# Optimization experiments

Measured on AMD Instinct MI355X. Metric: run time of the kernel, lower is better.

Reference implementation:

```python
import jax, jax.numpy as jnp
import numpy as np

PI = np.pi


def _apply_1q(state, gate, wire, n):
    # state: [B, 2**n] complex64; gate: [2,2] (shared) or [B,2,2] (per-sample)
    # PennyLane convention: wire 0 is the most-significant bit of the state index.
    B = state.shape[0]
    left, right = 2 ** wire, 2 ** (n - wire - 1)
    s = state.reshape(B, left, 2, right)
    if gate.ndim == 2:
        s = jnp.einsum('kl,balr->bakr', gate, s)
    else:
        s = jnp.einsum('bkl,balr->bakr', gate, s)
    return s.reshape(B, -1)


def _apply_cz(state, wire, n):
    # CZ on (wire, wire+1): flip sign of |..11..> amplitudes
    B = state.shape[0]
    left, right = 2 ** wire, 2 ** (n - wire - 2)
    s = state.reshape(B, left, 2, 2, right)
    s = s.at[:, :, 1, 1, :].multiply(-1.0)
    return s.reshape(B, -1)


def _ry_batched(theta):
    # theta: [B] -> [B,2,2] complex RY(theta)
    h = 0.5 * theta
    c, s = jnp.cos(h), jnp.sin(h)
    g = jnp.stack([jnp.stack([c, -s], -1), jnp.stack([s, c], -1)], -2)
    return g.astype(jnp.complex64)


def _rot(phi, theta, omega):
    # Rot = RZ(omega) @ RY(theta) @ RZ(phi)
    c, s = jnp.cos(0.5 * theta), jnp.sin(0.5 * theta)
    e_mm = jnp.exp(-0.5j * (phi + omega))
    e_pm = jnp.exp(0.5j * (phi - omega))
    e_mp = jnp.exp(-0.5j * (phi - omega))
    e_pp = jnp.exp(0.5j * (phi + omega))
    g = jnp.stack([jnp.stack([e_mm * c, -e_pm * s]), jnp.stack([e_mp * s, e_pp * c])])
    return g.astype(jnp.complex64)


def _simulate(enc, weights):
    # enc: [B, n_qubits] in [-1,1]; weights: [n_layers, n_qubits, 3]
    n_layers, n, _ = weights.shape
    B = enc.shape[0]
    state = jnp.zeros((B, 2 ** n), jnp.complex64).at[:, 0].set(1.0)
    ry = [_ry_batched(enc[:, i] * PI) for i in range(n)]
    for l in range(n_layers):
        for i in range(n):
            state = _apply_1q(state, ry[i], i, n)
        for i in range(n):
            state = _apply_1q(state, _rot(weights[l, i, 0], weights[l, i, 1], weights[l, i, 2]), i, n)
        for i in range(n - 1):
            state = _apply_cz(state, i, n)
    for i in range(n):
        state = _apply_1q(state, ry[i], i, n)
    probs = state.real ** 2 + state.imag ** 2  # [B, 2**n]
    # <Z_i> = sum_k probs[k] * (-1)^bit_i(k), wire 0 = MSB
    bits = (jnp.arange(2 ** n)[None, :] >> (n - 1 - jnp.arange(n))[:, None]) & 1
    signs = (1 - 2 * bits).astype(probs.dtype)  # [n, 2**n]
    return probs @ signs.T  # [B, n]


def setup_inputs() -> dict:
    B, D, NQ, NL, NA = 32768, 16, 8, 4, 4
    key = jax.random.key(0)
    ks = jax.random.split(key, 6)

    def lin(k, o, i):
        b = 1.0 / np.sqrt(i)
        k1, k2 = jax.random.split(k)
        return (jax.random.uniform(k1, (o, i), jnp.float32, -b, b),
                jax.random.uniform(k2, (o,), jnp.float32, -b, b))

    enc_w1, enc_b1 = lin(ks[1], 8, D)
    enc_w2, enc_b2 = lin(ks[2], NQ, 8)
    dec_w1, dec_b1 = lin(ks[3], 8, NQ)
    dec_w2, dec_b2 = lin(ks[4], NA, 8)
    q_weights = jax.random.uniform(ks[5], (NL, NQ, 3), jnp.float32, 0.0, 2.0 * PI)
    x = jax.random.normal(ks[0], (B, D), jnp.float32)
    return {"x": x, "enc_w1": enc_w1, "enc_b1": enc_b1, "enc_w2": enc_w2, "enc_b2": enc_b2,
            "q_weights": q_weights, "dec_w1": dec_w1, "dec_b1": dec_b1, "dec_w2": dec_w2, "dec_b2": dec_b2}


def reference(x, enc_w1, enc_b1, enc_w2, enc_b2, q_weights, dec_w1, dec_b1, dec_w2, dec_b2):
    h = jax.nn.relu(x @ enc_w1.T + enc_b1)
    enc = jnp.tanh(h @ enc_w2.T + enc_b2)          # [B, n_qubits]
    q = _simulate(enc, q_weights)                  # [B, n_qubits] PauliZ expvals
    h2 = jax.nn.relu(q @ dec_w1.T + dec_b1)
    return h2 @ dec_w2.T + dec_b2                  # [B, n_actions]
```

## Files before the change

### kernel.cpp

```cpp
#include <hip/hip_runtime.h>
#include <math.h>


#define PI_F 3.14159265358979323846f

struct C2 { float re, im; };

__device__ __forceinline__ C2 cmul(C2 a, C2 b) {
    C2 r;
    r.re = fmaf(a.re, b.re, -a.im * b.im);
    r.im = fmaf(a.re, b.im,  a.im * b.re);
    return r;
}

__device__ __forceinline__ float fxor(float x, int m) {
    return __int_as_float(__float_as_int(x) ^ m);
}

template<int CTRL>
__device__ __forceinline__ float dppf(float x) {
    int xi = __float_as_int(x);
    int r = __builtin_amdgcn_update_dpp(xi, xi, CTRL, 0xF, 0xF, false);
    return __int_as_float(r);
}
__device__ __forceinline__ float swz4(float x) {
    return __int_as_float(__builtin_amdgcn_ds_swizzle(__float_as_int(x), 0x101F));
}
template<int M>
__device__ __forceinline__ float lxor(float x) {
    if constexpr (M == 1)      return dppf<0xB1>(x);
    else if constexpr (M == 2) return dppf<0x4E>(x);
    else if constexpr (M == 4) return swz4(x);
    else                       return dppf<0x128>(x);
}

template<int M>
__device__ __forceinline__ void cross_gate(float cSr, float cSi, float cOr, float cOi,
                                           float sr[16], float si[16]) {
#pragma unroll
    for (int t = 0; t < 16; t++) {
        float pr = lxor<M>(sr[t]);
        float pi = lxor<M>(si[t]);
        float nr = fmaf(cSr, sr[t], fmaf(-cSi, si[t], fmaf(cOr, pr, -cOi * pi)));
        float ni = fmaf(cSr, si[t], fmaf( cSi, sr[t], fmaf(cOr, pi,  cOi * pr)));
        sr[t] = nr; si[t] = ni;
    }
}

template<int ST>
__device__ __forceinline__ void inlane_gate(float ar, float ai, float br, float bi,
                                            float sr[16], float si[16]) {
#pragma unroll
    for (int t = 0; t < 16; t++) {
        if ((t & ST) == 0) {
            const int u = t + ST;
            float xr = sr[t], xi = si[t], yr = sr[u], yi = si[u];
            sr[t] = fmaf(ar, xr, fmaf(-ai, xi, fmaf(-br, yr, -bi * yi)));
            si[t] = fmaf(ar, xi, fmaf( ai, xr, fmaf(-br, yi,  bi * yr)));
            sr[u] = fmaf(br, xr, fmaf(-bi, xi, fmaf( ar, yr,  ai * yi)));
            si[u] = fmaf(br, xi, fmaf( bi, xr, fmaf( ar, yi, -ai * yr)));
        }
    }
}

template<int M>
__device__ __forceinline__ void cross_ry(float c, float cO, float sr[16], float si[16]) {
#pragma unroll
    for (int t = 0; t < 16; t++) {
        float pr = lxor<M>(sr[t]);
        float pi = lxor<M>(si[t]);
        sr[t] = fmaf(c, sr[t], cO * pr);
        si[t] = fmaf(c, si[t], cO * pi);
    }
}
template<int ST>
__device__ __forceinline__ void inlane_ry(float c, float s, float sr[16], float si[16]) {
#pragma unroll
    for (int t = 0; t < 16; t++) {
        if ((t & ST) == 0) {
            const int u = t + ST;
            float xr = sr[t], xi = si[t], yr = sr[u], yi = si[u];
            sr[t] = fmaf(c, xr, -s * yr); si[t] = fmaf(c, xi, -s * yi);
            sr[u] = fmaf(s, xr,  c * yr); si[u] = fmaf(s, xi,  c * yi);
        }
    }
}

__device__ __forceinline__ void load_G2(const float* __restrict__ c_lds, int g,
                                        float cc, float ss,
                                        float& ar, float& ai, float& br, float& bi) {
    const float4 c0 = *(const float4*)(c_lds + 4 * g);
    ar = fmaf(c0.x, cc, -c0.z * ss);
    ai = fmaf(c0.y, cc,  c0.w * ss);
    br = fmaf(c0.z, cc,  c0.x * ss);
    bi = fmaf(c0.w, cc, -c0.y * ss);
}

__global__ __launch_bounds__(64) void qdqn_kernel(
    const float* __restrict__ x,
    const float* __restrict__ ew1, const float* __restrict__ eb1,
    const float* __restrict__ ew2, const float* __restrict__ eb2,
    const float* __restrict__ qw,
    const float* __restrict__ dw1, const float* __restrict__ db1,
    const float* __restrict__ dw2, const float* __restrict__ db2,
    float* __restrict__ out, int B, int NL) {
    __shared__ __align__(16) float c_lds[32 * 4];

    const int lane = threadIdx.x;
    const int n_gates = NL * 8;

    if (lane < n_gates) {
        const int g = lane;
        float phi = qw[3 * g + 0], th = qw[3 * g + 1], om = qw[3 * g + 2];
        float c = __cosf(0.5f * th), s = __sinf(0.5f * th);
        float A = 0.5f * (phi + om), Bb = 0.5f * (phi - om);
        float* o = c_lds + 4 * g;
        o[0] =  __cosf(A) * c;  o[1] = -__sinf(A) * c;
        o[2] =  __cosf(Bb) * s; o[3] = -__sinf(Bb) * s;
    }
    __syncthreads();

    const int L = lane & 15;
    int s = blockIdx.x * 4 + (lane >> 4);
    if (s >= B) s = B - 1;

    float xv[16];
    const float4* xp = (const float4*)(x + s * 16);
#pragma unroll
    for (int i = 0; i < 4; i++) {
        float4 v = xp[i];
        xv[4*i] = v.x; xv[4*i+1] = v.y; xv[4*i+2] = v.z; xv[4*i+3] = v.w;
    }
    float hbuf[8];
#pragma unroll
    for (int j = 0; j < 8; j++) {
        float a = eb1[j];
#pragma unroll
        for (int i = 0; i < 16; i++) a = fmaf(ew1[j * 16 + i], xv[i], a);
        hbuf[j] = fmaxf(a, 0.0f);
    }
    float cq[8], sq[8];
#pragma unroll
    for (int q = 0; q < 8; q++) {
        float a = eb2[q];
#pragma unroll
        for (int j = 0; j < 8; j++) a = fmaf(ew2[q * 8 + j], hbuf[j], a);
        float e = 1.0f - __fdividef(2.0f, __expf(2.0f * a) + 1.0f);
        float ang = e * (0.5f * PI_F);
        cq[q] = __cosf(ang);
        sq[q] = __sinf(ang);
    }

    int hiM[4], loM[4];
#pragma unroll
    for (int q = 0; q < 4; q++) {
        int hi = (L >> (3 - q)) & 1;
        hiM[q] = hi << 31;
        loM[q] = hiM[q] ^ 0x80000000;
    }

    const int L0 = L & 1, L1b = (L >> 1) & 1, L2b = (L >> 2) & 1, L3b = (L >> 3) & 1;
    const int cnt = (L3b & L2b) + (L2b & L1b) + (L1b & L0);
    const float mL = (cnt & 1) ? -1.0f : 1.0f;
    const float mH = L0 ? -mL : mL;
    constexpr bool CZNEG[16] =
        { false,false,false,true,  false,false,true,false,
          false,false,false,true,  true, true, false,true };

    float sr[16], si[16];
    {
        C2 P; P.re = 1.0f; P.im = 0.0f;
        C2 F[4][2];
#pragma unroll
        for (int q = 0; q < 8; q++) {
            float ar, ai, br, bi;
            load_G2(c_lds, q, cq[q], sq[q], ar, ai, br, bi);
            if (q < 4) {
                const bool hi = (L >> (3 - q)) & 1;
                C2 f; f.re = hi ? br : ar; f.im = hi ? bi : ai;
                P = cmul(P, f);
            } else {
                F[q-4][0].re = ar; F[q-4][0].im = ai;
                F[q-4][1].re = br; F[q-4][1].im = bi;
            }
        }
        C2 A0 = cmul(P, F[0][0]), A1 = cmul(P, F[0][1]);
        C2 Bv[4];
        Bv[0] = cmul(A0, F[1][0]); Bv[1] = cmul(A0, F[1][1]);
        Bv[2] = cmul(A1, F[1][0]); Bv[3] = cmul(A1, F[1][1]);
        C2 Cv[8];
#pragma unroll
        for (int i = 0; i < 8; i++) Cv[i] = cmul(Bv[i >> 1], F[2][i & 1]);
#pragma unroll
        for (int t = 0; t < 16; t++) {
            C2 v = cmul(Cv[t >> 1], F[3][t & 1]);
            float m = (t < 8) ? mL : mH;
            m = CZNEG[t] ? -m : m;
            sr[t] = v.re * m;
            si[t] = v.im * m;
        }
    }

    for (int l = 1; l < NL; l++) {
        const int g0 = l * 8;
        float ar, ai, br, bi;
        load_G2(c_lds, g0 + 0, cq[0], sq[0], ar, ai, br, bi);
        cross_gate<8>(ar, fxor(ai, hiM[0]), fxor(br, loM[0]), bi, sr, si);
        load_G2(c_lds, g0 + 1, cq[1], sq[1], ar, ai, br, bi);
        cross_gate<4>(ar, fxor(ai, hiM[1]), fxor(br, loM[1]), bi, sr, si);
        load_G2(c_lds, g0 + 2, cq[2], sq[2], ar, ai, br, bi);
        cross_gate<2>(ar, fxor(ai, hiM[2]), fxor(br, loM[2]), bi, sr, si);
        load_G2(c_lds, g0 + 3, cq[3], sq[3], ar, ai, br, bi);
        cross_gate<1>(ar, fxor(ai, hiM[3]), fxor(br, loM[3]), bi, sr, si);
        load_G2(c_lds, g0 + 4, cq[4], sq[4], ar, ai, br, bi);
        inlane_gate<8>(ar, ai, br, bi, sr, si);
        load_G2(c_lds, g0 + 5, cq[5], sq[5], ar, ai, br, bi);
        inlane_gate<4>(ar, ai, br, bi, sr, si);
        load_G2(c_lds, g0 + 6, cq[6], sq[6], ar, ai, br, bi);
        inlane_gate<2>(ar, ai, br, bi, sr, si);
        load_G2(c_lds, g0 + 7, cq[7], sq[7], ar, ai, br, bi);
        inlane_gate<1>(ar, ai, br, bi, sr, si);
#pragma unroll
        for (int t = 0; t < 16; t++) {
            float m = (t < 8) ? mL : mH;
            m = CZNEG[t] ? -m : m;
            sr[t] *= m; si[t] *= m;
        }
    }

    cross_ry<8>(cq[0], fxor(sq[0], loM[0]), sr, si);
    cross_ry<4>(cq[1], fxor(sq[1], loM[1]), sr, si);
    cross_ry<2>(cq[2], fxor(sq[2], loM[2]), sr, si);
    cross_ry<1>(cq[3], fxor(sq[3], loM[3]), sr, si);
    inlane_ry<8>(cq[4], sq[4], sr, si);
    inlane_ry<4>(cq[5], sq[5], sr, si);
    inlane_ry<2>(cq[6], sq[6], sr, si);
    inlane_ry<1>(cq[7], sq[7], sr, si);

    float p[16];
#pragma unroll
    for (int t = 0; t < 16; t++) p[t] = fmaf(sr[t], sr[t], si[t] * si[t]);

    float e0 = p[0]+p[1],  e1 = p[2]+p[3],  e2 = p[4]+p[5],  e3 = p[6]+p[7];
    float e4 = p[8]+p[9],  e5 = p[10]+p[11], e6 = p[12]+p[13], e7 = p[14]+p[15];
    float q0 = e0+e1, q1 = e2+e3, q2 = e4+e5, q3 = e6+e7;
    float h0 = q0+q1, h1 = q2+q3;
    float sumP = h0 + h1;

    float z[8];
#pragma unroll
    for (int w = 0; w < 4; w++)
        z[w] = ((L >> (3 - w)) & 1) ? -sumP : sumP;
    z[4] = h0 - h1;
    z[5] = (q0 - q1) + (q2 - q3);
    z[6] = (e0 - e1) + (e2 - e3) + (e4 - e5) + (e6 - e7);
    z[7] = (p[0]-p[1]) + (p[2]-p[3]) + (p[4]-p[5]) + (p[6]-p[7])
         + (p[8]-p[9]) + (p[10]-p[11]) + (p[12]-p[13]) + (p[14]-p[15]);

#pragma unroll
    for (int w = 0; w < 8; w++) z[w] += lxor<1>(z[w]);
#pragma unroll
    for (int w = 0; w < 8; w++) z[w] += lxor<2>(z[w]);
#pragma unroll
    for (int w = 0; w < 8; w++) z[w] += lxor<4>(z[w]);
#pragma unroll
    for (int w = 0; w < 8; w++) z[w] += lxor<8>(z[w]);

    float h2[8];
#pragma unroll
    for (int j = 0; j < 8; j++) {
        float a = db1[j];
#pragma unroll
        for (int w = 0; w < 8; w++) a = fmaf(dw1[j * 8 + w], z[w], a);
        h2[j] = fmaxf(a, 0.0f);
    }
    if (L < 4) {
        float a = db2[L];
#pragma unroll
        for (int j = 0; j < 8; j++) a = fmaf(dw2[L * 8 + j], h2[j], a);
        out[s * 4 + L] = a;
    }
}

extern "C" void kernel_launch(void* const* d_in, const int* in_sizes, int n_in,
                              void* d_out, int out_size, void* d_ws, size_t ws_size,
                              hipStream_t stream) {
    const float* x   = (const float*)d_in[0];
    const float* ew1 = (const float*)d_in[1];
    const float* eb1 = (const float*)d_in[2];
    const float* ew2 = (const float*)d_in[3];
    const float* eb2 = (const float*)d_in[4];
    const float* qw  = (const float*)d_in[5];
    const float* dw1 = (const float*)d_in[6];
    const float* db1 = (const float*)d_in[7];
    const float* dw2 = (const float*)d_in[8];
    const float* db2 = (const float*)d_in[9];
    float* out = (float*)d_out;

    int B = in_sizes[0] / 16;
    int n_gates = in_sizes[5] / 3;
    int NL = n_gates / 8;

    int blocks = (B + 3) / 4;
    qdqn_kernel<<<blocks, 64, 0, stream>>>(x, ew1, eb1, ew2, eb2, qw,
                                           dw1, db1, dw2, db2, out, B, NL);
}
```

Baseline: 137.1 us.

## Replace cross-lane gates with LDS transposes and packed-FP32 in-lane SU2 updates

```diff
diff --git a/kernel.cpp b/kernel.cpp
--- a/kernel.cpp
+++ b/kernel.cpp
@@ -4,8 +4,9 @@
 
 #define PI_F 3.14159265358979323846f
 
+typedef float v2f __attribute__((ext_vector_type(2)));
+
 struct C2 { float re, im; };
-
 __device__ __forceinline__ C2 cmul(C2 a, C2 b) {
     C2 r;
     r.re = fmaf(a.re, b.re, -a.im * b.im);
@@ -13,8 +14,27 @@
     return r;
 }
 
-__device__ __forceinline__ float fxor(float x, int m) {
-    return __int_as_float(__float_as_int(x) ^ m);
+__device__ __forceinline__ v2f pk_mul(v2f a, v2f b) {
+    v2f d; asm("v_pk_mul_f32 %0, %1, %2" : "=v"(d) : "v"(a), "v"(b)); return d;
+}
+__device__ __forceinline__ v2f pk_mul_neg(v2f a, v2f b) {
+    v2f d; asm("v_pk_mul_f32 %0, %1, %2 neg_lo:[1,0] neg_hi:[1,0]"
+               : "=v"(d) : "v"(a), "v"(b)); return d;
+}
+__device__ __forceinline__ v2f pk_fma(v2f a, v2f b, v2f c) {
+    v2f d; asm("v_pk_fma_f32 %0, %1, %2, %3" : "=v"(d) : "v"(a), "v"(b), "v"(c)); return d;
+}
+__device__ __forceinline__ v2f pk_fma_nn(v2f a, v2f b, v2f c) {
+    v2f d; asm("v_pk_fma_f32 %0, %1, %2, %3 neg_lo:[1,0,0] neg_hi:[1,0,0]"
+               : "=v"(d) : "v"(a), "v"(b), "v"(c)); return d;
+}
+__device__ __forceinline__ v2f pk_fma_swl(v2f a, v2f b, v2f c) {
+    v2f d; asm("v_pk_fma_f32 %0, %1, %2, %3 op_sel:[0,1,0] op_sel_hi:[1,0,1] neg_lo:[1,0,0]"
+               : "=v"(d) : "v"(a), "v"(b), "v"(c)); return d;
+}
+__device__ __forceinline__ v2f pk_fma_swh(v2f a, v2f b, v2f c) {
+    v2f d; asm("v_pk_fma_f32 %0, %1, %2, %3 op_sel:[0,1,0] op_sel_hi:[1,0,1] neg_hi:[1,0,0]"
+               : "=v"(d) : "v"(a), "v"(b), "v"(c)); return d;
 }
 
 template<int CTRL>
@@ -23,80 +43,66 @@
     int r = __builtin_amdgcn_update_dpp(xi, xi, CTRL, 0xF, 0xF, false);
     return __int_as_float(r);
 }
-__device__ __forceinline__ float swz4(float x) {
-    return __int_as_float(__builtin_amdgcn_ds_swizzle(__float_as_int(x), 0x101F));
-}
 template<int M>
 __device__ __forceinline__ float lxor(float x) {
     if constexpr (M == 1)      return dppf<0xB1>(x);
     else if constexpr (M == 2) return dppf<0x4E>(x);
-    else if constexpr (M == 4) return swz4(x);
+    else if constexpr (M == 4) return __int_as_float(
+        __builtin_amdgcn_ds_swizzle(__float_as_int(x), 0x101F));
     else                       return dppf<0x128>(x);
 }
 
-template<int M>
-__device__ __forceinline__ void cross_gate(float cSr, float cSi, float cOr, float cOi,
-                                           float sr[16], float si[16]) {
-#pragma unroll
-    for (int t = 0; t < 16; t++) {
-        float pr = lxor<M>(sr[t]);
-        float pi = lxor<M>(si[t]);
-        float nr = fmaf(cSr, sr[t], fmaf(-cSi, si[t], fmaf(cOr, pr, -cOi * pi)));
-        float ni = fmaf(cSr, si[t], fmaf( cSi, sr[t], fmaf(cOr, pi,  cOi * pr)));
-        sr[t] = nr; si[t] = ni;
-    }
+__device__ __forceinline__ void build_G(const float* __restrict__ c_lds, int g,
+                                        float cc, float ss,
+                                        v2f& arr, v2f& aii, v2f& brr, v2f& bii) {
+    const float4 c0 = *(const float4*)(c_lds + 4 * g);
+    float ar = fmaf(c0.x, cc, -c0.z * ss);
+    float ai = fmaf(c0.y, cc,  c0.w * ss);
+    float br = fmaf(c0.z, cc,  c0.x * ss);
+    float bi = fmaf(c0.w, cc, -c0.y * ss);
+    arr = (v2f){ar, ar}; aii = (v2f){ai, ai};
+    brr = (v2f){br, br}; bii = (v2f){bi, bi};
 }
 
 template<int ST>
-__device__ __forceinline__ void inlane_gate(float ar, float ai, float br, float bi,
-                                            float sr[16], float si[16]) {
+__device__ __forceinline__ void su2_inlane(v2f arr, v2f aii, v2f brr, v2f bii,
+                                           v2f z[16]) {
 #pragma unroll
     for (int t = 0; t < 16; t++) {
         if ((t & ST) == 0) {
             const int u = t + ST;
-            float xr = sr[t], xi = si[t], yr = sr[u], yi = si[u];
-            sr[t] = fmaf(ar, xr, fmaf(-ai, xi, fmaf(-br, yr, -bi * yi)));
-            si[t] = fmaf(ar, xi, fmaf( ai, xr, fmaf(-br, yi,  bi * yr)));
-            sr[u] = fmaf(br, xr, fmaf(-bi, xi, fmaf( ar, yr,  ai * yi)));
-            si[u] = fmaf(br, xi, fmaf( bi, xr, fmaf( ar, yi, -ai * yr)));
-        }
-    }
-}
-
-template<int M>
-__device__ __forceinline__ void cross_ry(float c, float cO, float sr[16], float si[16]) {
-#pragma unroll
-    for (int t = 0; t < 16; t++) {
-        float pr = lxor<M>(sr[t]);
-        float pi = lxor<M>(si[t]);
-        sr[t] = fmaf(c, sr[t], cO * pr);
-        si[t] = fmaf(c, si[t], cO * pi);
-    }
-}
+            v2f x = z[t], y = z[u];
+            v2f nx = pk_mul(arr, x);
+            nx = pk_fma_swl(aii, x, nx);
+            nx = pk_fma_nn (brr, y, nx);
+            nx = pk_fma_swl(bii, y, nx);
+            v2f ny = pk_mul(brr, x);
+            ny = pk_fma_swl(bii, x, ny);
+            ny = pk_fma   (arr, y, ny);
+            ny = pk_fma_swh(aii, y, ny);
+            z[t] = nx; z[u] = ny;
+        }
+    }
+}
+
 template<int ST>
-__device__ __forceinline__ void inlane_ry(float c, float s, float sr[16], float si[16]) {
+__device__ __forceinline__ void ry_inlane(v2f cc, v2f ss, v2f z[16]) {
 #pragma unroll
     for (int t = 0; t < 16; t++) {
         if ((t & ST) == 0) {
             const int u = t + ST;
-            float xr = sr[t], xi = si[t], yr = sr[u], yi = si[u];
-            sr[t] = fmaf(c, xr, -s * yr); si[t] = fmaf(c, xi, -s * yi);
-            sr[u] = fmaf(s, xr,  c * yr); si[u] = fmaf(s, xi,  c * yi);
-        }
-    }
-}
-
-__device__ __forceinline__ void load_G2(const float* __restrict__ c_lds, int g,
-                                        float cc, float ss,
-                                        float& ar, float& ai, float& br, float& bi) {
-    const float4 c0 = *(const float4*)(c_lds + 4 * g);
-    ar = fmaf(c0.x, cc, -c0.z * ss);
-    ai = fmaf(c0.y, cc,  c0.w * ss);
-    br = fmaf(c0.z, cc,  c0.x * ss);
-    bi = fmaf(c0.w, cc, -c0.y * ss);
-}
-
-__global__ __launch_bounds__(64) void qdqn_kernel(
+            v2f x = z[t], y = z[u];
+            z[t] = pk_fma_nn(ss, y, pk_mul(cc, x));
+            z[u] = pk_fma   (cc, y, pk_mul(ss, x));
+        }
+    }
+}
+
+__device__ __constant__ const bool CZNEG[16] =
+    { false,false,false,true,  false,false,true,false,
+      false,false,false,true,  true, true, false,true };
+
+__global__ __launch_bounds__(128) void qdqn_kernel(
     const float* __restrict__ x,
     const float* __restrict__ ew1, const float* __restrict__ eb1,
     const float* __restrict__ ew2, const float* __restrict__ eb2,
@@ -105,12 +111,13 @@
     const float* __restrict__ dw2, const float* __restrict__ db2,
     float* __restrict__ out, int B, int NL) {
     __shared__ __align__(16) float c_lds[32 * 4];
-
-    const int lane = threadIdx.x;
+    __shared__ __align__(16) v2f tbuf[2 * 4 * 288];
+
+    const int tid = threadIdx.x;
     const int n_gates = NL * 8;
 
-    if (lane < n_gates) {
-        const int g = lane;
+    if (tid < n_gates) {
+        const int g = tid;
         float phi = qw[3 * g + 0], th = qw[3 * g + 1], om = qw[3 * g + 2];
         float c = __cosf(0.5f * th), s = __sinf(0.5f * th);
         float A = 0.5f * (phi + om), Bb = 0.5f * (phi - om);
@@ -120,9 +127,13 @@
     }
     __syncthreads();
 
+    const int wave = tid >> 6;
+    const int lane = tid & 63;
+    const int grp = lane >> 4;
     const int L = lane & 15;
-    int s = blockIdx.x * 4 + (lane >> 4);
+    int s = blockIdx.x * 8 + wave * 4 + grp;
     if (s >= B) s = B - 1;
+    v2f* tb = &tbuf[(wave * 4 + grp) * 288];
 
     float xv[16];
     const float4* xp = (const float4*)(x + s * 16);
@@ -151,30 +162,24 @@
         sq[q] = __sinf(ang);
     }
 
-    int hiM[4], loM[4];
-#pragma unroll
-    for (int q = 0; q < 4; q++) {
-        int hi = (L >> (3 - q)) & 1;
-        hiM[q] = hi << 31;
-        loM[q] = hiM[q] ^ 0x80000000;
-    }
-
     const int L0 = L & 1, L1b = (L >> 1) & 1, L2b = (L >> 2) & 1, L3b = (L >> 3) & 1;
     const int cnt = (L3b & L2b) + (L2b & L1b) + (L1b & L0);
     const float mL = (cnt & 1) ? -1.0f : 1.0f;
     const float mH = L0 ? -mL : mL;
-    constexpr bool CZNEG[16] =
-        { false,false,false,true,  false,false,true,false,
-          false,false,false,true,  true, true, false,true };
-
-    float sr[16], si[16];
+    const float mO = L3b ? -mL : mL;
+    const v2f mL2 = (v2f){mL, mL}, mH2 = (v2f){mH, mH}, mO2 = (v2f){mO, mO};
+
+    v2f z[16];
     {
         C2 P; P.re = 1.0f; P.im = 0.0f;
         C2 F[4][2];
 #pragma unroll
         for (int q = 0; q < 8; q++) {
-            float ar, ai, br, bi;
-            load_G2(c_lds, q, cq[q], sq[q], ar, ai, br, bi);
+            const float4 c0 = *(const float4*)(c_lds + 4 * q);
+            float ar = fmaf(c0.x, cq[q], -c0.z * sq[q]);
+            float ai = fmaf(c0.y, cq[q],  c0.w * sq[q]);
+            float br = fmaf(c0.z, cq[q],  c0.x * sq[q]);
+            float bi = fmaf(c0.w, cq[q], -c0.y * sq[q]);
             if (q < 4) {
                 const bool hi = (L >> (3 - q)) & 1;
                 C2 f; f.re = hi ? br : ar; f.im = hi ? bi : ai;
@@ -196,50 +201,97 @@
             C2 v = cmul(Cv[t >> 1], F[3][t & 1]);
             float m = (t < 8) ? mL : mH;
             m = CZNEG[t] ? -m : m;
-            sr[t] = v.re * m;
-            si[t] = v.im * m;
-        }
-    }
-
+            z[t].x = v.re * m;
+            z[t].y = v.im * m;
+        }
+    }
+
+    auto transpose = [&]() {
+        float4* wrow = (float4*)(tb + L * 18);
+#pragma unroll
+        for (int k = 0; k < 8; k++)
+            wrow[k] = make_float4(z[2*k].x, z[2*k].y, z[2*k+1].x, z[2*k+1].y);
+        __builtin_amdgcn_wave_barrier();
+#pragma unroll
+        for (int j = 0; j < 16; j++) z[j] = tb[j * 18 + L];
+        __builtin_amdgcn_wave_barrier();
+    };
+
+    auto cz_A = [&]() {
+#pragma unroll
+        for (int t = 0; t < 16; t++) {
+            v2f m = (t < 8) ? mL2 : mH2;
+            z[t] = CZNEG[t] ? pk_mul_neg(m, z[t]) : pk_mul(m, z[t]);
+        }
+    };
+    auto cz_B = [&]() {
+#pragma unroll
+        for (int j = 0; j < 16; j++) {
+            v2f m = (j & 1) ? mO2 : mL2;
+            z[j] = CZNEG[j] ? pk_mul_neg(m, z[j]) : pk_mul(m, z[j]);
+        }
+    };
+
+    v2f arr, aii, brr, bii;
+    bool inB = false;
     for (int l = 1; l < NL; l++) {
         const int g0 = l * 8;
-        float ar, ai, br, bi;
-        load_G2(c_lds, g0 + 0, cq[0], sq[0], ar, ai, br, bi);
-        cross_gate<8>(ar, fxor(ai, hiM[0]), fxor(br, loM[0]), bi, sr, si);
-        load_G2(c_lds, g0 + 1, cq[1], sq[1], ar, ai, br, bi);
-        cross_gate<4>(ar, fxor(ai, hiM[1]), fxor(br, loM[1]), bi, sr, si);
-        load_G2(c_lds, g0 + 2, cq[2], sq[2], ar, ai, br, bi);
-        cross_gate<2>(ar, fxor(ai, hiM[2]), fxor(br, loM[2]), bi, sr, si);
-        load_G2(c_lds, g0 + 3, cq[3], sq[3], ar, ai, br, bi);
-        cross_gate<1>(ar, fxor(ai, hiM[3]), fxor(br, loM[3]), bi, sr, si);
-        load_G2(c_lds, g0 + 4, cq[4], sq[4], ar, ai, br, bi);
-        inlane_gate<8>(ar, ai, br, bi, sr, si);
-        load_G2(c_lds, g0 + 5, cq[5], sq[5], ar, ai, br, bi);
-        inlane_gate<4>(ar, ai, br, bi, sr, si);
-        load_G2(c_lds, g0 + 6, cq[6], sq[6], ar, ai, br, bi);
-        inlane_gate<2>(ar, ai, br, bi, sr, si);
-        load_G2(c_lds, g0 + 7, cq[7], sq[7], ar, ai, br, bi);
-        inlane_gate<1>(ar, ai, br, bi, sr, si);
-#pragma unroll
-        for (int t = 0; t < 16; t++) {
-            float m = (t < 8) ? mL : mH;
-            m = CZNEG[t] ? -m : m;
-            sr[t] *= m; si[t] *= m;
-        }
-    }
-
-    cross_ry<8>(cq[0], fxor(sq[0], loM[0]), sr, si);
-    cross_ry<4>(cq[1], fxor(sq[1], loM[1]), sr, si);
-    cross_ry<2>(cq[2], fxor(sq[2], loM[2]), sr, si);
-    cross_ry<1>(cq[3], fxor(sq[3], loM[3]), sr, si);
-    inlane_ry<8>(cq[4], sq[4], sr, si);
-    inlane_ry<4>(cq[5], sq[5], sr, si);
-    inlane_ry<2>(cq[6], sq[6], sr, si);
-    inlane_ry<1>(cq[7], sq[7], sr, si);
+        if (!inB) {
+            build_G(c_lds, g0+4, cq[4], sq[4], arr, aii, brr, bii); su2_inlane<8>(arr, aii, brr, bii, z);
+            build_G(c_lds, g0+5, cq[5], sq[5], arr, aii, brr, bii); su2_inlane<4>(arr, aii, brr, bii, z);
+            build_G(c_lds, g0+6, cq[6], sq[6], arr, aii, brr, bii); su2_inlane<2>(arr, aii, brr, bii, z);
+            build_G(c_lds, g0+7, cq[7], sq[7], arr, aii, brr, bii); su2_inlane<1>(arr, aii, brr, bii, z);
+            transpose();
+            build_G(c_lds, g0+0, cq[0], sq[0], arr, aii, brr, bii); su2_inlane<8>(arr, aii, brr, bii, z);
+            build_G(c_lds, g0+1, cq[1], sq[1], arr, aii, brr, bii); su2_inlane<4>(arr, aii, brr, bii, z);
+            build_G(c_lds, g0+2, cq[2], sq[2], arr, aii, brr, bii); su2_inlane<2>(arr, aii, brr, bii, z);
+            build_G(c_lds, g0+3, cq[3], sq[3], arr, aii, brr, bii); su2_inlane<1>(arr, aii, brr, bii, z);
+            cz_B();
+            inB = true;
+        } else {
+            build_G(c_lds, g0+0, cq[0], sq[0], arr, aii, brr, bii); su2_inlane<8>(arr, aii, brr, bii, z);
+            build_G(c_lds, g0+1, cq[1], sq[1], arr, aii, brr, bii); su2_inlane<4>(arr, aii, brr, bii, z);
+            build_G(c_lds, g0+2, cq[2], sq[2], arr, aii, brr, bii); su2_inlane<2>(arr, aii, brr, bii, z);
+            build_G(c_lds, g0+3, cq[3], sq[3], arr, aii, brr, bii); su2_inlane<1>(arr, aii, brr, bii, z);
+            transpose();
+            build_G(c_lds, g0+4, cq[4], sq[4], arr, aii, brr, bii); su2_inlane<8>(arr, aii, brr, bii, z);
+            build_G(c_lds, g0+5, cq[5], sq[5], arr, aii, brr, bii); su2_inlane<4>(arr, aii, brr, bii, z);
+            build_G(c_lds, g0+6, cq[6], sq[6], arr, aii, brr, bii); su2_inlane<2>(arr, aii, brr, bii, z);
+            build_G(c_lds, g0+7, cq[7], sq[7], arr, aii, brr, bii); su2_inlane<1>(arr, aii, brr, bii, z);
+            cz_A();
+            inB = false;
+        }
+    }
+
+    {
+        v2f cc, ss;
+        if (inB) {
+            cc=(v2f){cq[0],cq[0]}; ss=(v2f){sq[0],sq[0]}; ry_inlane<8>(cc, ss, z);
+            cc=(v2f){cq[1],cq[1]}; ss=(v2f){sq[1],sq[1]}; ry_inlane<4>(cc, ss, z);
+            cc=(v2f){cq[2],cq[2]}; ss=(v2f){sq[2],sq[2]}; ry_inlane<2>(cc, ss, z);
+            cc=(v2f){cq[3],cq[3]}; ss=(v2f){sq[3],sq[3]}; ry_inlane<1>(cc, ss, z);
+            transpose();
+            cc=(v2f){cq[4],cq[4]}; ss=(v2f){sq[4],sq[4]}; ry_inlane<8>(cc, ss, z);
+            cc=(v2f){cq[5],cq[5]}; ss=(v2f){sq[5],sq[5]}; ry_inlane<4>(cc, ss, z);
+            cc=(v2f){cq[6],cq[6]}; ss=(v2f){sq[6],sq[6]}; ry_inlane<2>(cc, ss, z);
+            cc=(v2f){cq[7],cq[7]}; ss=(v2f){sq[7],sq[7]}; ry_inlane<1>(cc, ss, z);
+        } else {
+            cc=(v2f){cq[4],cq[4]}; ss=(v2f){sq[4],sq[4]}; ry_inlane<8>(cc, ss, z);
+            cc=(v2f){cq[5],cq[5]}; ss=(v2f){sq[5],sq[5]}; ry_inlane<4>(cc, ss, z);
+            cc=(v2f){cq[6],cq[6]}; ss=(v2f){sq[6],sq[6]}; ry_inlane<2>(cc, ss, z);
+            cc=(v2f){cq[7],cq[7]}; ss=(v2f){sq[7],sq[7]}; ry_inlane<1>(cc, ss, z);
+            transpose();
+            cc=(v2f){cq[0],cq[0]}; ss=(v2f){sq[0],sq[0]}; ry_inlane<8>(cc, ss, z);
+            cc=(v2f){cq[1],cq[1]}; ss=(v2f){sq[1],sq[1]}; ry_inlane<4>(cc, ss, z);
+            cc=(v2f){cq[2],cq[2]}; ss=(v2f){sq[2],sq[2]}; ry_inlane<2>(cc, ss, z);
+            cc=(v2f){cq[3],cq[3]}; ss=(v2f){sq[3],sq[3]}; ry_inlane<1>(cc, ss, z);
+            transpose();
+        }
+    }
 
     float p[16];
 #pragma unroll
-    for (int t = 0; t < 16; t++) p[t] = fmaf(sr[t], sr[t], si[t] * si[t]);
+    for (int t = 0; t < 16; t++) p[t] = fmaf(z[t].x, z[t].x, z[t].y * z[t].y);
 
     float e0 = p[0]+p[1],  e1 = p[2]+p[3],  e2 = p[4]+p[5],  e3 = p[6]+p[7];
     float e4 = p[8]+p[9],  e5 = p[10]+p[11], e6 = p[12]+p[13], e7 = p[14]+p[15];
@@ -247,31 +299,31 @@
     float h0 = q0+q1, h1 = q2+q3;
     float sumP = h0 + h1;
 
-    float z[8];
+    float zv[8];
 #pragma unroll
     for (int w = 0; w < 4; w++)
-        z[w] = ((L >> (3 - w)) & 1) ? -sumP : sumP;
-    z[4] = h0 - h1;
-    z[5] = (q0 - q1) + (q2 - q3);
-    z[6] = (e0 - e1) + (e2 - e3) + (e4 - e5) + (e6 - e7);
-    z[7] = (p[0]-p[1]) + (p[2]-p[3]) + (p[4]-p[5]) + (p[6]-p[7])
-         + (p[8]-p[9]) + (p[10]-p[11]) + (p[12]-p[13]) + (p[14]-p[15]);
-
-#pragma unroll
-    for (int w = 0; w < 8; w++) z[w] += lxor<1>(z[w]);
-#pragma unroll
-    for (int w = 0; w < 8; w++) z[w] += lxor<2>(z[w]);
-#pragma unroll
-    for (int w = 0; w < 8; w++) z[w] += lxor<4>(z[w]);
-#pragma unroll
-    for (int w = 0; w < 8; w++) z[w] += lxor<8>(z[w]);
+        zv[w] = ((L >> (3 - w)) & 1) ? -sumP : sumP;
+    zv[4] = h0 - h1;
+    zv[5] = (q0 - q1) + (q2 - q3);
+    zv[6] = (e0 - e1) + (e2 - e3) + (e4 - e5) + (e6 - e7);
+    zv[7] = (p[0]-p[1]) + (p[2]-p[3]) + (p[4]-p[5]) + (p[6]-p[7])
+          + (p[8]-p[9]) + (p[10]-p[11]) + (p[12]-p[13]) + (p[14]-p[15]);
+
+#pragma unroll
+    for (int w = 0; w < 8; w++) zv[w] += lxor<1>(zv[w]);
+#pragma unroll
+    for (int w = 0; w < 8; w++) zv[w] += lxor<2>(zv[w]);
+#pragma unroll
+    for (int w = 0; w < 8; w++) zv[w] += lxor<4>(zv[w]);
+#pragma unroll
+    for (int w = 0; w < 8; w++) zv[w] += lxor<8>(zv[w]);
 
     float h2[8];
 #pragma unroll
     for (int j = 0; j < 8; j++) {
         float a = db1[j];
 #pragma unroll
-        for (int w = 0; w < 8; w++) a = fmaf(dw1[j * 8 + w], z[w], a);
+        for (int w = 0; w < 8; w++) a = fmaf(dw1[j * 8 + w], zv[w], a);
         h2[j] = fmaxf(a, 0.0f);
     }
     if (L < 4) {
@@ -301,7 +353,7 @@
     int n_gates = in_sizes[5] / 3;
     int NL = n_gates / 8;
 
-    int blocks = (B + 3) / 4;
-    qdqn_kernel<<<blocks, 64, 0, stream>>>(x, ew1, eb1, ew2, eb2, qw,
-                                           dw1, db1, dw2, db2, out, B, NL);
-}
+    int blocks = (B + 7) / 8;
+    qdqn_kernel<<<blocks, 128, 0, stream>>>(x, ew1, eb1, ew2, eb2, qw,
+                                            dw1, db1, dw2, db2, out, B, NL);
+}
```

New measurement: 121.6 us. 1.13x faster.
